# Performance work log

Hardware: AMD Instinct MI355X
Metric: run time of the kernel (lower is better)

The kernel has to match this reference:

```python
import jax, jax.numpy as jnp
import numpy as np

# Mamba2Simple defaults for Mamba2Simple(768, headdim=64)
D_MODEL = 768
D_STATE = 128
D_CONV = 4
EXPAND = 2
HEADDIM = 64
D_INNER = EXPAND * D_MODEL           # 1536
NHEADS = D_INNER // HEADDIM          # 24
CONV_DIM = D_INNER + 2 * D_STATE     # 1792 (x, B, C share the depthwise conv)
D_IN_PROJ = 2 * D_INNER + 2 * D_STATE + NHEADS  # 3352 (z, xBC, dt)
N_LAYERS = 4
IM8 = 64      # 8x8 image tokens
IM64 = 4096   # 64x64 image tokens
L = 1 + IM8 + IM64  # 4161 = s0 + im8 + zoom(im8)
B = 4
EPS = 1e-5


def setup_inputs() -> dict:
    key = jax.random.key(0)
    ks = iter(jax.random.split(key, 40))
    nrm = lambda shape, s=0.02: jax.random.normal(next(ks), shape, jnp.float32) * s
    inp = {
        'im8': jax.random.normal(next(ks), (B, IM8, 3), jnp.float32),
        'im64': jax.random.normal(next(ks), (B, IM64, 3), jnp.float32),
        # RGBToModel / ModelToRGB linear projections
        'from_rgb_w': nrm((3, D_MODEL)),
        'from_rgb_b': jnp.zeros((D_MODEL,), jnp.float32),
        'to_rgb_w': nrm((D_MODEL, 3)),
        'to_rgb_b': jnp.zeros((3,), jnp.float32),
        # learned prefix token and zoom positional suffix
        's0': nrm((1, 1, D_MODEL), 1.0),
        'suffix': nrm((IM64, D_MODEL), 1.0),
        'norm0_w': jnp.ones((D_MODEL,), jnp.float32),
        'norm0_b': jnp.zeros((D_MODEL,), jnp.float32),
        # per-layer (stacked over N_LAYERS) Mamba2 params
        'ln_w': jnp.ones((N_LAYERS, D_MODEL), jnp.float32),
        'ln_b': jnp.zeros((N_LAYERS, D_MODEL), jnp.float32),
        'in_proj_w': nrm((N_LAYERS, D_MODEL, D_IN_PROJ)),
        'conv_w': nrm((N_LAYERS, CONV_DIM, D_CONV), 0.1),
        'conv_b': jnp.zeros((N_LAYERS, CONV_DIM), jnp.float32),
        'dt_bias': nrm((N_LAYERS, NHEADS), 0.1),
        'A_log': jnp.log(jax.random.uniform(next(ks), (N_LAYERS, NHEADS), jnp.float32, 1.0, 16.0)),
        'D': nrm((N_LAYERS, NHEADS), 1.0),
        'gn_w': jnp.ones((N_LAYERS, D_INNER), jnp.float32),
        'out_proj_w': nrm((N_LAYERS, D_INNER, D_MODEL)),
    }
    return inp


def _layernorm(x, w, b):
    mu = jnp.mean(x, axis=-1, keepdims=True)
    var = jnp.mean((x - mu) ** 2, axis=-1, keepdims=True)
    return (x - mu) * jax.lax.rsqrt(var + EPS) * w + b


def _rmsnorm(x, w):
    return x * jax.lax.rsqrt(jnp.mean(x * x, axis=-1, keepdims=True) + EPS) * w


def _causal_conv1d(x, w, b):
    # x: (B, L, C) depthwise causal conv, kernel (C, K)
    xt = x.transpose(0, 2, 1)  # (B, C, L)
    y = jax.lax.conv_general_dilated(
        xt, w[:, None, :], window_strides=(1,), padding=[(D_CONV - 1, 0)],
        dimension_numbers=('NCH', 'OIH', 'NCH'), feature_group_count=w.shape[0])
    return y.transpose(0, 2, 1) + b


def _mamba2(u, Wi, cw, cb, dtb, Alog, Dh, gw, Wo):
    # u: (B, L, d_model)
    Bsz, Ln, _ = u.shape
    zxbcdt = u @ Wi  # (B, L, D_IN_PROJ)
    z = zxbcdt[..., :D_INNER]
    xBC = zxbcdt[..., D_INNER:D_INNER + CONV_DIM]
    dt = jax.nn.softplus(zxbcdt[..., D_INNER + CONV_DIM:] + dtb)  # (B, L, H)
    xBC = jax.nn.silu(_causal_conv1d(xBC, cw, cb))
    x = xBC[..., :D_INNER].reshape(Bsz, Ln, NHEADS, HEADDIM)  # (B,L,H,P)
    Bm = xBC[..., D_INNER:D_INNER + D_STATE]                  # (B,L,N)
    Cm = xBC[..., D_INNER + D_STATE:]                         # (B,L,N)
    A = -jnp.exp(Alog)            # (H,)
    dA = jnp.exp(dt * A)          # (B,L,H) decay factors

    def step(state, inputs):
        # state: (B,H,P,N)
        xt, dtt, dAt, Bt, Ct = inputs
        state = state * dAt[:, :, None, None] + jnp.einsum('bh,bhp,bn->bhpn', dtt, xt, Bt)
        y = jnp.einsum('bhpn,bn->bhp', state, Ct)
        return state, y

    st0 = jnp.zeros((Bsz, NHEADS, HEADDIM, D_STATE), u.dtype)
    xs = (x.transpose(1, 0, 2, 3), dt.transpose(1, 0, 2), dA.transpose(1, 0, 2),
          Bm.transpose(1, 0, 2), Cm.transpose(1, 0, 2))
    _, ys = jax.lax.scan(step, st0, xs)  # ys: (L,B,H,P)
    y = ys.transpose(1, 0, 2, 3) + Dh[None, None, :, None] * x  # D skip per head
    y = y.reshape(Bsz, Ln, D_INNER)
    y = _rmsnorm(y * jax.nn.silu(z), gw)  # RMSNormGated (norm_before_gate=False)
    return y @ Wo


def reference(im8, im64, from_rgb_w, from_rgb_b, to_rgb_w, to_rgb_b, s0, suffix,
              norm0_w, norm0_b, ln_w, ln_b, in_proj_w, conv_w, conv_b,
              dt_bias, A_log, D, gn_w, out_proj_w):
    Bsz = im8.shape[0]
    h8 = im8 @ from_rgb_w + from_rgb_b  # (B,64,d)
    # zoom: each 8x8 pixel repeated into an 8x8 block -> 64x64, plus suffix
    v = h8.reshape(Bsz, 8, 8, D_MODEL)
    zm = jnp.repeat(jnp.repeat(v, 8, axis=1), 8, axis=2).reshape(Bsz, IM64, D_MODEL) + suffix
    x = jnp.concatenate([jnp.broadcast_to(s0, (Bsz, 1, D_MODEL)), h8, zm], axis=1)  # (B,4161,d)
    x = _layernorm(x, norm0_w, norm0_b)
    for i in range(N_LAYERS):
        x = x + _mamba2(_layernorm(x, ln_w[i], ln_b[i]), in_proj_w[i], conv_w[i],
                        conv_b[i], dt_bias[i], A_log[i], D[i], gn_w[i], out_proj_w[i])
    x = x[:, -IM64:]
    y_hat = x @ to_rgb_w + to_rgb_b  # (B,4096,3)
    loss = jnp.mean((y_hat - im64) ** 2)
    return y_hat, loss
```

## Files before the change

kernel.cpp:

```cpp
#include <hip/hip_runtime.h>
#include <hip/hip_bf16.h>
#include <math.h>

#define LTOT 4161
#define BATCH 4
#define NROWS (BATCH*LTOT)
#define NPAD1 3456
#define DM 768
#define DI 1536
#define DIP 3352
#define ZLD 3328
#define NH 24
#define HD 64
#define DS 128
#define EPSF 1e-5f
#define CHK 128
#define NCH 33
#define NBLK (BATCH*NCH*NH)
#define LDF 136
#define XLD 72
#define RLD 264

typedef __attribute__((ext_vector_type(8))) __bf16 bf16x8;
typedef __attribute__((ext_vector_type(4))) float f32x4;
typedef __attribute__((ext_vector_type(8))) short short8;
typedef __attribute__((ext_vector_type(4))) unsigned int u32x4;
typedef unsigned short u16;
typedef unsigned int u32;

static __device__ __forceinline__ u16 f2bf(float f){
  unsigned u = __builtin_bit_cast(unsigned, f);
  u += 0x7FFFu + ((u >> 16) & 1u);
  return (u16)(u >> 16);
}
static __device__ __forceinline__ float bf2f(u16 v){
  return __builtin_bit_cast(float, ((unsigned)v) << 16);
}
static __device__ __forceinline__ float siluf(float v){ return v / (1.f + __expf(-v)); }

static __device__ __forceinline__ int xcd_swz(int orig, int nwg){
  int xcd = orig & 7;
  int idx = orig >> 3;
  int q = nwg >> 3, r = nwg & 7;
  int base = (xcd < r) ? xcd*(q + 1) : r*(q + 1) + (xcd - r)*q;
  return base + idx;
}

__device__ __forceinline__ float blockSum256(float v, float* sh){
  #pragma unroll
  for (int o = 32; o > 0; o >>= 1) v += __shfl_down(v, o);
  int w = threadIdx.x >> 6;
  if ((threadIdx.x & 63) == 0) sh[w] = v;
  __syncthreads();
  v = sh[0] + sh[1] + sh[2] + sh[3];
  __syncthreads();
  return v;
}

__global__ __launch_bounds__(256)
void build_x_kernel(const float* __restrict__ im8, const float* __restrict__ frw,
                    const float* __restrict__ frb, const float* __restrict__ s0,
                    const float* __restrict__ suffix, const float* __restrict__ w,
                    const float* __restrict__ bb, float* __restrict__ x)
{
  int row = blockIdx.x;
  int b = row / LTOT, l = row % LTOT;
  int t = threadIdx.x;
  __shared__ float sh[4];
  float v[3];
  if (l == 0) {
    #pragma unroll
    for (int i = 0; i < 3; i++) v[i] = s0[t + i*256];
  } else if (l <= 64) {
    int p = l - 1;
    float r0 = im8[(b*64 + p)*3 + 0], r1 = im8[(b*64 + p)*3 + 1], r2 = im8[(b*64 + p)*3 + 2];
    #pragma unroll
    for (int i = 0; i < 3; i++) {
      int d = t + i*256;
      v[i] = r0*frw[d] + r1*frw[768 + d] + r2*frw[1536 + d] + frb[d];
    }
  } else {
    int j = l - 65;
    int p = ((j >> 9) << 3) | ((j & 63) >> 3);
    float r0 = im8[(b*64 + p)*3 + 0], r1 = im8[(b*64 + p)*3 + 1], r2 = im8[(b*64 + p)*3 + 2];
    #pragma unroll
    for (int i = 0; i < 3; i++) {
      int d = t + i*256;
      v[i] = r0*frw[d] + r1*frw[768 + d] + r2*frw[1536 + d] + frb[d] + suffix[(size_t)j*768 + d];
    }
  }
  float s = v[0] + v[1] + v[2];
  s = blockSum256(s, sh);
  float mu = s * (1.f/768.f);
  float q = 0;
  #pragma unroll
  for (int i = 0; i < 3; i++) { float d = v[i] - mu; q += d*d; }
  q = blockSum256(q, sh);
  float rs = rsqrtf(q * (1.f/768.f) + EPSF);
  float* xr = x + (size_t)row*DM;
  #pragma unroll
  for (int i = 0; i < 3; i++) {
    int d = t + i*256;
    xr[d] = (v[i] - mu)*rs*w[d] + bb[d];
  }
}

__global__ __launch_bounds__(256)
void ln_bf16_kernel(const float* __restrict__ x, const float* __restrict__ w,
                    const float* __restrict__ bb, u16* __restrict__ out,
                    float* __restrict__ ssq)
{
  int row = blockIdx.x;
  int t = threadIdx.x;
  __shared__ float sh[4];
  const float* xr = x + (size_t)row*DM;
  float v[3];
  #pragma unroll
  for (int i = 0; i < 3; i++) v[i] = xr[t + i*256];
  if (t == 0) ssq[row] = 0.f;
  float s = v[0] + v[1] + v[2];
  s = blockSum256(s, sh);
  float mu = s * (1.f/768.f);
  float q = 0;
  #pragma unroll
  for (int i = 0; i < 3; i++) { float d = v[i] - mu; q += d*d; }
  q = blockSum256(q, sh);
  float rs = rsqrtf(q * (1.f/768.f) + EPSF);
  u16* orow = out + (size_t)row*DM;
  #pragma unroll
  for (int i = 0; i < 3; i++) {
    int d = t + i*256;
    orow[d] = f2bf((v[i] - mu)*rs*w[d] + bb[d]);
  }
}

__global__ __launch_bounds__(256)
void transp_bf16(const float* __restrict__ in, u16* __restrict__ out, int K, int N)
{
  __shared__ float tl[32][33];
  int tx = threadIdx.x & 31, ty = threadIdx.x >> 5;
  int n0 = blockIdx.x * 32, k0 = blockIdx.y * 32;
  #pragma unroll
  for (int r = 0; r < 4; r++) {
    int k = k0 + ty + r*8, n = n0 + tx;
    tl[ty + r*8][tx] = (n < N) ? in[(size_t)k*N + n] : 0.f;
  }
  __syncthreads();
  #pragma unroll
  for (int r = 0; r < 4; r++) {
    int n = n0 + ty + r*8, k = k0 + tx;
    out[(size_t)n*K + k] = f2bf(tl[tx][ty + r*8]);
  }
}

#define LD8(p) (*(const short8*)(p))

__global__ __launch_bounds__(256)
void gemm0(const u16* __restrict__ A, const u16* __restrict__ BT,
           u16* __restrict__ zxO, const float* __restrict__ dtbias,
           float* __restrict__ dtO)
{
  __shared__ __align__(16) u16 As[2][128*40];
  __shared__ __align__(16) u16 Bs[2][128*40];
  const int t = threadIdx.x;
  const int nid = xcd_swz(blockIdx.y*27 + blockIdx.x, 27*131);
  const int bm = nid / 27, bn = nid % 27;
  const int lane = t & 63, wave = t >> 6;
  const int wr = wave >> 1, wc = wave & 1;
  const int r16 = lane & 15, kb = lane >> 4;

  const int m = t >> 1, half = t & 1;
  const int grow = bm*128 + m;
  const bool valid = grow < NROWS;
  const u16* gA = A + (size_t)(valid ? grow : 0)*DM + half*16;
  const u16* gB = BT + (size_t)(bn*128 + m)*DM + half*16;
  const int wofs = m*40 + half*16;

  short8 a0 = {}, a1 = {}, b0, b1;
  b0 = LD8(gB); b1 = LD8(gB + 8);
  if (valid) { a0 = LD8(gA); a1 = LD8(gA + 8); }
  *(short8*)&As[0][wofs] = a0; *(short8*)&As[0][wofs + 8] = a1;
  *(short8*)&Bs[0][wofs] = b0; *(short8*)&Bs[0][wofs + 8] = b1;
  __syncthreads();

  f32x4 acc[4][4] = {};
  int p = 0;
  for (int kt = 0; kt < DM; kt += 32) {
    const bool more = (kt + 32 < DM);
    if (more) {
      b0 = LD8(gB + kt + 32); b1 = LD8(gB + kt + 40);
      if (valid) { a0 = LD8(gA + kt + 32); a1 = LD8(gA + kt + 40); }
    }
    bf16x8 af[4], bfr[4];
    #pragma unroll
    for (int i = 0; i < 4; i++) af[i]  = *(const bf16x8*)&As[p][(wr*64 + i*16 + r16)*40 + kb*8];
    #pragma unroll
    for (int i = 0; i < 4; i++) bfr[i] = *(const bf16x8*)&Bs[p][(wc*64 + i*16 + r16)*40 + kb*8];
    #pragma unroll
    for (int i = 0; i < 4; i++)
      #pragma unroll
      for (int j = 0; j < 4; j++)
        acc[i][j] = __builtin_amdgcn_mfma_f32_16x16x32_bf16(af[i], bfr[j], acc[i][j], 0, 0, 0);
    if (more) {
      *(short8*)&As[p^1][wofs] = a0; *(short8*)&As[p^1][wofs + 8] = a1;
      *(short8*)&Bs[p^1][wofs] = b0; *(short8*)&Bs[p^1][wofs + 8] = b1;
    }
    __syncthreads();
    p ^= 1;
  }
  const int rbase = bm*128 + wr*64, cbase = bn*128 + wc*64;
  #pragma unroll
  for (int i = 0; i < 4; i++) {
    #pragma unroll
    for (int j = 0; j < 4; j++) {
      int col = cbase + j*16 + r16;
      #pragma unroll
      for (int e = 0; e < 4; e++) {
        int row = rbase + i*16 + kb*4 + e;
        if (row < NROWS) {
          float v = acc[i][j][e];
          if (col < ZLD) {
            zxO[(size_t)row*ZLD + col] = f2bf(v);
          } else if (col < DIP) {
            int hh = col - ZLD;
            float d = v + dtbias[hh];
            d = (d > 20.f) ? d : log1pf(expf(d));
            dtO[(size_t)row*NH + hh] = d;
          }
        }
      }
    }
  }
}

__global__ __launch_bounds__(256)
void gemm_out(const u16* __restrict__ A, const float* __restrict__ ssq,
              const float* __restrict__ gw, const u16* __restrict__ BT,
              float* __restrict__ X)
{
  __shared__ __align__(16) u16 As[2][128*40];
  __shared__ __align__(16) u16 Bs[2][128*40];
  __shared__ float gwl[DI];
  const int t = threadIdx.x;
  const int nid = xcd_swz(blockIdx.y*6 + blockIdx.x, 6*131);
  const int bm = nid / 6, bn = nid % 6;
  const int lane = t & 63, wave = t >> 6;
  const int wr = wave >> 1, wc = wave & 1;
  const int r16 = lane & 15, kb = lane >> 4;

  for (int i = t; i < DI; i += 256) gwl[i] = gw[i];

  const int m = t >> 1, half = t & 1;
  const int grow = bm*128 + m;
  const bool valid = grow < NROWS;
  const float rs = valid ? rsqrtf(ssq[grow] * (1.f/1536.f) + EPSF) : 0.f;
  const u16* gA = A + (size_t)(valid ? grow : 0)*ZLD + half*16;
  const u16* gB = BT + (size_t)(bn*128 + m)*DI + half*16;
  const int wofs = m*40 + half*16;

  short8 ra0 = {}, ra1 = {}, b0, b1;
  b0 = LD8(gB); b1 = LD8(gB + 8);
  if (valid) { ra0 = LD8(gA); ra1 = LD8(gA + 8); }
  __syncthreads();
  {
    const int c0 = half*16;
    short8 ta0, ta1;
    #pragma unroll
    for (int j = 0; j < 8; j++) ta0[j] = (short)f2bf(bf2f((u16)ra0[j]) * rs * gwl[c0 + j]);
    #pragma unroll
    for (int j = 0; j < 8; j++) ta1[j] = (short)f2bf(bf2f((u16)ra1[j]) * rs * gwl[c0 + 8 + j]);
    *(short8*)&As[0][wofs] = ta0; *(short8*)&As[0][wofs + 8] = ta1;
    *(short8*)&Bs[0][wofs] = b0;  *(short8*)&Bs[0][wofs + 8] = b1;
  }
  __syncthreads();

  f32x4 acc[4][4] = {};
  int p = 0;
  for (int kt = 0; kt < DI; kt += 32) {
    const bool more = (kt + 32 < DI);
    if (more) {
      b0 = LD8(gB + kt + 32); b1 = LD8(gB + kt + 40);
      if (valid) { ra0 = LD8(gA + kt + 32); ra1 = LD8(gA + kt + 40); }
    }
    bf16x8 af[4], bfr[4];
    #pragma unroll
    for (int i = 0; i < 4; i++) af[i]  = *(const bf16x8*)&As[p][(wr*64 + i*16 + r16)*40 + kb*8];
    #pragma unroll
    for (int i = 0; i < 4; i++) bfr[i] = *(const bf16x8*)&Bs[p][(wc*64 + i*16 + r16)*40 + kb*8];
    #pragma unroll
    for (int i = 0; i < 4; i++)
      #pragma unroll
      for (int j = 0; j < 4; j++)
        acc[i][j] = __builtin_amdgcn_mfma_f32_16x16x32_bf16(af[i], bfr[j], acc[i][j], 0, 0, 0);
    if (more) {
      const int c0 = kt + 32 + half*16;
      short8 ta0, ta1;
      #pragma unroll
      for (int j = 0; j < 8; j++) ta0[j] = (short)f2bf(bf2f((u16)ra0[j]) * rs * gwl[c0 + j]);
      #pragma unroll
      for (int j = 0; j < 8; j++) ta1[j] = (short)f2bf(bf2f((u16)ra1[j]) * rs * gwl[c0 + 8 + j]);
      *(short8*)&As[p^1][wofs] = ta0; *(short8*)&As[p^1][wofs + 8] = ta1;
      *(short8*)&Bs[p^1][wofs] = b0;  *(short8*)&Bs[p^1][wofs + 8] = b1;
    }
    __syncthreads();
    p ^= 1;
  }
  const int rbase = bm*128 + wr*64, cbase = bn*128 + wc*64;
  #pragma unroll
  for (int i = 0; i < 4; i++) {
    #pragma unroll
    for (int j = 0; j < 4; j++) {
      int col = cbase + j*16 + r16;
      #pragma unroll
      for (int e = 0; e < 4; e++) {
        int row = rbase + i*16 + kb*4 + e;
        if (row < NROWS) X[(size_t)row*DM + col] += acc[i][j][e];
      }
    }
  }
}


__global__ __launch_bounds__(128)
void dtcs_kernel(const float* __restrict__ dt, const float* __restrict__ alog,
                 float* __restrict__ csb, float* __restrict__ dtvb,
                 float* __restrict__ wjsb, float* __restrict__ dtot)
{
  const int id = blockIdx.x;
  const int h = id % NH; const int c = (id / NH) % NCH; const int b = id / (NH*NCH);
  const int t = threadIdx.x;
  const int base = c*CHK;
  int rows = LTOT - base; if (rows > CHK) rows = CHK;
  __shared__ float cs[128];
  float dv = 0.f;
  if (t < rows) dv = dt[(size_t)(b*LTOT + base + t)*NH + h];
  const float aexp = __expf(alog[h]);
  cs[t] = -dv * aexp;
  __syncthreads();
  for (int off = 1; off < 128; off <<= 1) {
    float add = (t >= off) ? cs[t - off] : 0.f;
    __syncthreads();
    cs[t] += add;
    __syncthreads();
  }
  float csl = cs[127];
  size_t o = (size_t)id*128 + t;
  csb[o] = cs[t];
  dtvb[o] = dv;
  wjsb[o] = __expf(csl - cs[t]) * dv;
  if (t == 0) dtot[id] = __expf(csl);
}

__global__ __launch_bounds__(256)
void convBC_kernel(const u16* __restrict__ zx, const float* __restrict__ cw,
                   const float* __restrict__ cb, u16* __restrict__ Ccv,
                   u16* __restrict__ BcvT, u16* __restrict__ Sraw)
{
  const int bc = xcd_swz(blockIdx.x, BATCH*NCH);
  const int b = bc / NCH, c = bc % NCH;
  const int t = threadIdx.x;
  const int base = c*CHK;
  __shared__ __align__(16) u16 raw[131*RLD + 8];
  __shared__ __align__(16) u16 Bt[128*LDF];
  __shared__ __align__(16) u16 Ct[128*LDF];
  const u16* zb = zx + (size_t)(b*LTOT)*ZLD;

  #pragma unroll
  for (int rg = 0; rg < 17; rg++) {
    int idx = rg*256 + t;
    int r = idx >> 5, seg = idx & 31;
    if (r < 131) {
      int g = base - 3 + r;
      short8 v = {};
      if (g >= 0 && g < LTOT) v = LD8(zb + (size_t)g*ZLD + 3072 + seg*8);
      *(short8*)&raw[r*RLD + seg*8] = v;
    }
  }
  __syncthreads();
  {
    const int isC = t >> 7, n = t & 127;
    const int ch = 1536 + t;
    float w0 = cw[ch*4+0], w1 = cw[ch*4+1], w2 = cw[ch*4+2], w3 = cw[ch*4+3];
    float bias = cb[ch];
    float r0 = bf2f(raw[0*RLD + t]);
    float r1 = bf2f(raw[1*RLD + t]);
    float r2 = bf2f(raw[2*RLD + t]);
    u16* dstT = isC ? Ct : Bt;
    #pragma unroll 4
    for (int j = 0; j < 128; j++) {
      float r3 = bf2f(raw[(j + 3)*RLD + t]);
      float o = bias + w0*r0 + w1*r1 + w2*r2 + w3*r3;
      dstT[j*LDF + n] = f2bf(siluf(o));
      r0 = r1; r1 = r2; r2 = r3;
    }
  }
  __syncthreads();
  #pragma unroll
  for (int rg = 0; rg < 8; rg++) {
    int idx = rg*256 + t;
    int r = idx >> 4, seg = idx & 15;
    int g = base + r;
    if (g < LTOT)
      *(short8*)(Ccv + (size_t)(b*LTOT + g)*128 + seg*8) = *(const short8*)&Ct[r*LDF + seg*8];
  }
  u16* bT = BcvT + (size_t)bc*16384;
  #pragma unroll
  for (int rg = 0; rg < 8; rg++) {
    int idx = rg*256 + t;
    int n = idx >> 4, js = (idx & 15)*8;
    short8 v;
    #pragma unroll
    for (int k = 0; k < 8; k++) v[k] = (short)Bt[(js + k)*LDF + n];
    *(short8*)(bT + n*128 + js) = v;
  }
  {
    const int lane = t & 63, wave = t >> 6;
    const int r16 = lane & 15, kb = lane >> 4;
    f32x4 acc[2][8] = {};
    #pragma unroll
    for (int kt = 0; kt < 4; kt++) {
      bf16x8 af[2], bfr[8];
      #pragma unroll
      for (int m2 = 0; m2 < 2; m2++) af[m2] = *(const bf16x8*)&Ct[(wave*32 + m2*16 + r16)*LDF + kt*32 + kb*8];
      #pragma unroll
      for (int nj = 0; nj < 8; nj++) bfr[nj] = *(const bf16x8*)&Bt[(nj*16 + r16)*LDF + kt*32 + kb*8];
      #pragma unroll
      for (int m2 = 0; m2 < 2; m2++)
        #pragma unroll
        for (int nj = 0; nj < 8; nj++)
          acc[m2][nj] = __builtin_amdgcn_mfma_f32_16x16x32_bf16(af[m2], bfr[nj], acc[m2][nj], 0, 0, 0);
    }
    u16* sdst = Sraw + (size_t)bc*16384;
    #pragma unroll
    for (int m2 = 0; m2 < 2; m2++)
      #pragma unroll
      for (int nj = 0; nj < 8; nj++)
        #pragma unroll
        for (int e = 0; e < 4; e++) {
          int i = wave*32 + m2*16 + kb*4 + e;
          int j = nj*16 + r16;
          sdst[i*128 + j] = f2bf(acc[m2][nj][e]);
        }
  }
}

__global__ __launch_bounds__(256)
void chunk_state_kernel(const u16* __restrict__ zx, const float* __restrict__ wjsb,
                        const float* __restrict__ cw, const float* __restrict__ cb,
                        const u16* __restrict__ BcvT, u16* __restrict__ cstat)
{
  const int id = xcd_swz(blockIdx.x, NBLK);
  const int h = id % NH; const int c = (id / NH) % NCH; const int b = id / (NH*NCH);
  const int t = threadIdx.x;
  const int base = c*CHK;

  __shared__ __align__(16) u16 Bbuf[128*LDF];
  __shared__ __align__(16) u16 xbuf[131*XLD + 8];
  __shared__ float wjs[128];

  const u16* zb = zx + (size_t)(b*LTOT)*ZLD;
  if (t < 128) wjs[t] = wjsb[(size_t)id*128 + t];
  {
    const u16* bT = BcvT + (size_t)(b*NCH + c)*16384;
    #pragma unroll
    for (int rg = 0; rg < 8; rg++) {
      int idx = rg*256 + t;
      int n = idx >> 4, js = (idx & 15)*8;
      *(short8*)&Bbuf[n*LDF + js] = LD8(bT + n*128 + js);
    }
  }
  #pragma unroll
  for (int rg = 0; rg < 5; rg++) {
    int r = rg*32 + (t >> 3);
    int seg = t & 7;
    if (r < 131) {
      int g = base - 3 + r;
      short8 v = {};
      if (g >= 0 && g < LTOT) v = LD8(zb + (size_t)g*ZLD + 1536 + h*HD + seg*8);
      *(short8*)&xbuf[r*XLD + seg*8] = v;
    }
  }
  __syncthreads();

  const int p_ = t & 63, jq = t >> 6;
  u32 pkx[16];
  {
    const int ch = h*HD + p_;
    float w0 = cw[ch*4+0], w1 = cw[ch*4+1], w2 = cw[ch*4+2], w3 = cw[ch*4+3];
    float bias = cb[ch];
    const int rb = jq*32;
    float r0 = bf2f(xbuf[(rb+0)*XLD + p_]);
    float r1 = bf2f(xbuf[(rb+1)*XLD + p_]);
    float r2 = bf2f(xbuf[(rb+2)*XLD + p_]);
    #pragma unroll
    for (int k2 = 0; k2 < 16; k2++) {
      float r3 = bf2f(xbuf[(rb + 2*k2 + 3)*XLD + p_]);
      float o0 = bias + w0*r0 + w1*r1 + w2*r2 + w3*r3;
      float r4 = bf2f(xbuf[(rb + 2*k2 + 4)*XLD + p_]);
      float o1 = bias + w0*r1 + w1*r2 + w2*r3 + w3*r4;
      float s0 = siluf(o0) * wjs[rb + 2*k2];
      float s1 = siluf(o1) * wjs[rb + 2*k2 + 1];
      pkx[k2] = (u32)f2bf(s0) | ((u32)f2bf(s1) << 16);
      r0 = r2; r1 = r3; r2 = r4;
    }
  }
  __syncthreads();
  #pragma unroll
  for (int q = 0; q < 4; q++) {
    u32x4 v; v[0] = pkx[q*4]; v[1] = pkx[q*4+1]; v[2] = pkx[q*4+2]; v[3] = pkx[q*4+3];
    *(u32x4*)&xbuf[p_*LDF + jq*32 + q*8] = v;
  }
  __syncthreads();

  const int lane = t & 63, wave = t >> 6;
  const int r16 = lane & 15, kb = lane >> 4;
  const int n0 = wave*32;
  f32x4 acc[4][2] = {};
  #pragma unroll
  for (int kt = 0; kt < 4; kt++) {
    bf16x8 af[4], bfr[2];
    #pragma unroll
    for (int m = 0; m < 4; m++) af[m] = *(const bf16x8*)&xbuf[(m*16 + r16)*LDF + kt*32 + kb*8];
    #pragma unroll
    for (int nn = 0; nn < 2; nn++) bfr[nn] = *(const bf16x8*)&Bbuf[(n0 + nn*16 + r16)*LDF + kt*32 + kb*8];
    #pragma unroll
    for (int m = 0; m < 4; m++)
      #pragma unroll
      for (int nn = 0; nn < 2; nn++)
        acc[m][nn] = __builtin_amdgcn_mfma_f32_16x16x32_bf16(af[m], bfr[nn], acc[m][nn], 0, 0, 0);
  }
  u16* dst = cstat + (size_t)id*64*128;
  #pragma unroll
  for (int m = 0; m < 4; m++)
    #pragma unroll
    for (int nn = 0; nn < 2; nn++)
      #pragma unroll
      for (int e = 0; e < 4; e++) {
        int p = m*16 + kb*4 + e;
        int n = n0 + nn*16 + r16;
        dst[p*128 + n] = f2bf(acc[m][nn][e]);
      }
}

__global__ __launch_bounds__(256)
void state_scan_kernel(u16* __restrict__ cstat, const float* __restrict__ dtot)
{
  const int b = blockIdx.x / NH, h = blockIdx.x % NH;
  const int t = threadIdx.x;
  float run[32];
  #pragma unroll
  for (int k = 0; k < 32; k++) run[k] = 0.f;
  size_t id0 = (size_t)(b*NCH)*NH + h;
  short8 cur[4];
  {
    const u16* s0 = cstat + id0*8192 + t*32;
    #pragma unroll
    for (int q = 0; q < 4; q++) cur[q] = LD8(s0 + q*8);
  }
  float d = dtot[id0];
  for (int c = 0; c < NCH; ++c) {
    size_t id = (size_t)(b*NCH + c)*NH + h;
    u16* slab = cstat + id*8192 + t*32;
    short8 nxt[4] = {}; float nd = 0.f;
    if (c + 1 < NCH) {
      const u16* sn = slab + (size_t)NH*8192;
      #pragma unroll
      for (int q = 0; q < 4; q++) nxt[q] = LD8(sn + q*8);
      nd = dtot[id + NH];
    }
    short8 out[4];
    #pragma unroll
    for (int q = 0; q < 4; q++)
      #pragma unroll
      for (int k = 0; k < 8; k++) {
        int idx = q*8 + k;
        float csv = bf2f((u16)cur[q][k]);
        out[q][k] = (short)f2bf(run[idx]);
        run[idx] = run[idx]*d + csv;
      }
    #pragma unroll
    for (int q = 0; q < 4; q++) *(short8*)(slab + q*8) = out[q];
    #pragma unroll
    for (int q = 0; q < 4; q++) cur[q] = nxt[q];
    d = nd;
  }
}

__global__ __launch_bounds__(512, 4)
void chunk_output_kernel(u16* __restrict__ zx, const float* __restrict__ csb,
                         const float* __restrict__ dtvb, const float* __restrict__ cw,
                         const float* __restrict__ cb, const float* __restrict__ Dvec,
                         const u16* __restrict__ Sraw, const u16* __restrict__ Ccv,
                         const u16* __restrict__ cstat, float* __restrict__ ssq)
{
  const int id = xcd_swz(blockIdx.x, NBLK);
  const int h = id % NH; const int c = (id / NH) % NCH; const int b = id / (NH*NCH);
  const int t = threadIdx.x;
  const int base = c*CHK;
  int rows = LTOT - base; if (rows > CHK) rows = CHK;

  __shared__ __align__(16) u16 Bc[128*LDF];
  __shared__ __align__(16) u16 stT[64*LDF];
  __shared__ __align__(16) u16 xbuf[131*XLD + 8];
  __shared__ float dtv[128];
  __shared__ float cs[128];

  const u16* zb = zx + (size_t)(b*LTOT)*ZLD;
  const size_t crow0 = (size_t)(b*LTOT)*128;
  if (t < 128) {
    cs[t]  = csb[(size_t)id*128 + t];
    dtv[t] = dtvb[(size_t)id*128 + t];
  }
  {
    const u16* slab = cstat + (size_t)id*8192;
    int p = t >> 3, nb = (t & 7)*16;
    *(short8*)&stT[p*LDF + nb]     = LD8(slab + p*128 + nb);
    *(short8*)&stT[p*LDF + nb + 8] = LD8(slab + p*128 + nb + 8);
  }
  #pragma unroll
  for (int rg = 0; rg < 3; rg++) {
    int r = rg*64 + (t >> 3);
    int seg = t & 7;
    if (r < 131) {
      int g = base - 3 + r;
      short8 v = {};
      if (g >= 0 && g < LTOT) v = LD8(zb + (size_t)g*ZLD + 1536 + h*HD + seg*8);
      *(short8*)&xbuf[r*XLD + seg*8] = v;
    }
  }
  __syncthreads();

  const int p_ = t & 63, jq = t >> 6;
  u32 pkx[8];
  {
    const int ch = h*HD + p_;
    float w0 = cw[ch*4+0], w1 = cw[ch*4+1], w2 = cw[ch*4+2], w3 = cw[ch*4+3];
    float bias = cb[ch];
    const int rb = jq*16;
    float r0 = bf2f(xbuf[(rb+0)*XLD + p_]);
    float r1 = bf2f(xbuf[(rb+1)*XLD + p_]);
    float r2 = bf2f(xbuf[(rb+2)*XLD + p_]);
    #pragma unroll
    for (int k2 = 0; k2 < 8; k2++) {
      float r3 = bf2f(xbuf[(rb + 2*k2 + 3)*XLD + p_]);
      float o0 = bias + w0*r0 + w1*r1 + w2*r2 + w3*r3;
      float r4 = bf2f(xbuf[(rb + 2*k2 + 4)*XLD + p_]);
      float o1 = bias + w0*r1 + w1*r2 + w2*r3 + w3*r4;
      int j0 = rb + 2*k2;
      u32 lo = (j0     < rows) ? (u32)f2bf(siluf(o0)) : 0u;
      u32 hi = (j0 + 1 < rows) ? (u32)f2bf(siluf(o1)) : 0u;
      pkx[k2] = lo | (hi << 16);
      r0 = r2; r1 = r3; r2 = r4;
    }
  }
  {
    const u16* sS = Sraw + (size_t)(b*NCH + c)*16384;
    #pragma unroll
    for (int q = 0; q < 4; q++) {
      int idx = q*512 + t;
      int i = idx >> 4, seg = (idx & 15)*8;
      short8 s = LD8(sS + i*128 + seg);
      float csi = cs[i];
      short8 o;
      #pragma unroll
      for (int k = 0; k < 8; k++) {
        int j = seg + k;
        float f = 0.f;
        if (j <= i && i < rows) f = __expf(csi - cs[j]) * dtv[j];
        o[k] = (short)f2bf(bf2f((u16)s[k]) * f);
      }
      *(short8*)&Bc[i*LDF + seg] = o;
    }
  }
  __syncthreads();
  {
    u32x4 v0; v0[0] = pkx[0]; v0[1] = pkx[1]; v0[2] = pkx[2]; v0[3] = pkx[3];
    u32x4 v1; v1[0] = pkx[4]; v1[1] = pkx[5]; v1[2] = pkx[6]; v1[3] = pkx[7];
    *(u32x4*)&xbuf[p_*LDF + jq*16]     = v0;
    *(u32x4*)&xbuf[p_*LDF + jq*16 + 8] = v1;
  }
  __syncthreads();

  const int lane = t & 63, wave = t >> 6;
  const int r16 = lane & 15, kb = lane >> 4;

  {
    const int iq = wave;
    bf16x8 cF[4];
    {
      int i = iq*16 + r16;
      int g = base + i; if (g >= LTOT) g = base;
      #pragma unroll
      for (int kt = 0; kt < 4; kt++)
        cF[kt] = *(const bf16x8*)(Ccv + crow0 + (size_t)g*128 + kt*32 + kb*8);
    }
    f32x4 accY[4] = {};
    #pragma unroll
    for (int kt = 0; kt < 4; kt++) {
      bf16x8 af = *(const bf16x8*)&Bc[(iq*16 + r16)*LDF + kt*32 + kb*8];
      #pragma unroll
      for (int n = 0; n < 4; n++) {
        bf16x8 bfr = *(const bf16x8*)&xbuf[(n*16 + r16)*LDF + kt*32 + kb*8];
        accY[n] = __builtin_amdgcn_mfma_f32_16x16x32_bf16(af, bfr, accY[n], 0, 0, 0);
      }
    }
    f32x4 accS[4] = {};
    #pragma unroll
    for (int kt = 0; kt < 4; kt++) {
      #pragma unroll
      for (int n = 0; n < 4; n++) {
        bf16x8 bfr = *(const bf16x8*)&stT[(n*16 + r16)*LDF + kt*32 + kb*8];
        accS[n] = __builtin_amdgcn_mfma_f32_16x16x32_bf16(cF[kt], bfr, accS[n], 0, 0, 0);
      }
    }
    const float dcoef = Dvec[h];
    #pragma unroll
    for (int e = 0; e < 4; e++) {
      int i = iq*16 + kb*4 + e;
      if (i < rows) {
        float sc = __expf(cs[i]);
        size_t orow = (size_t)(b*LTOT + base + i)*ZLD + h*HD;
        float g2 = 0.f;
        #pragma unroll
        for (int n = 0; n < 4; n++) {
          int p = n*16 + r16;
          float xv = bf2f(xbuf[p*LDF + i]);
          float yv = accY[n][e] + sc*accS[n][e] + dcoef*xv;
          float gv = yv * siluf(bf2f(zx[orow + p]));
          zx[orow + p] = f2bf(gv);
          g2 += gv*gv;
        }
        g2 += __shfl_xor(g2, 1);
        g2 += __shfl_xor(g2, 2);
        g2 += __shfl_xor(g2, 4);
        g2 += __shfl_xor(g2, 8);
        if (r16 == 0) atomicAdd(&ssq[b*LTOT + base + i], g2);
      }
    }
  }
}

__global__ __launch_bounds__(256)
void head_kernel(const float* __restrict__ x, const float* __restrict__ tw,
                 const float* __restrict__ tb, const float* __restrict__ im64,
                 float* __restrict__ out, float* __restrict__ partial)
{
  int bj = blockIdx.x;
  int b = bj >> 12, j = bj & 4095;
  int row = b*LTOT + 65 + j;
  const float* xr = x + (size_t)row*DM;
  int t = threadIdx.x;
  float p0 = 0, p1 = 0, p2 = 0;
  for (int k = t; k < 768; k += 256) {
    float xv = xr[k];
    p0 += xv*tw[k*3 + 0]; p1 += xv*tw[k*3 + 1]; p2 += xv*tw[k*3 + 2];
  }
  __shared__ float sh[4];
  p0 = blockSum256(p0, sh);
  p1 = blockSum256(p1, sh);
  p2 = blockSum256(p2, sh);
  if (t == 0) {
    float y0 = p0 + tb[0], y1 = p1 + tb[1], y2 = p2 + tb[2];
    size_t o = (size_t)bj*3;
    out[o] = y0; out[o + 1] = y1; out[o + 2] = y2;
    float d0 = y0 - im64[o], d1 = y1 - im64[o + 1], d2 = y2 - im64[o + 2];
    partial[bj] = d0*d0 + d1*d1 + d2*d2;
  }
}

__global__ __launch_bounds__(256)
void loss_reduce(const float* __restrict__ partial, float* __restrict__ out)
{
  int t = threadIdx.x;
  float s = 0.f;
  for (int i = t; i < BATCH*4096; i += 256) s += partial[i];
  __shared__ float sh[4];
  s = blockSum256(s, sh);
  if (t == 0) out[49152] = s * (1.f/49152.f);
}

static inline size_t alignup(size_t v){ return (v + 255) & ~(size_t)255; }

extern "C" void kernel_launch(void* const* d_in, const int* in_sizes, int n_in,
                              void* d_out, int out_size, void* d_ws, size_t ws_size,
                              hipStream_t stream)
{
  const float* im8        = (const float*)d_in[0];
  const float* im64       = (const float*)d_in[1];
  const float* from_rgb_w = (const float*)d_in[2];
  const float* from_rgb_b = (const float*)d_in[3];
  const float* to_rgb_w   = (const float*)d_in[4];
  const float* to_rgb_b   = (const float*)d_in[5];
  const float* s0         = (const float*)d_in[6];
  const float* suffix     = (const float*)d_in[7];
  const float* norm0_w    = (const float*)d_in[8];
  const float* norm0_b    = (const float*)d_in[9];
  const float* ln_w       = (const float*)d_in[10];
  const float* ln_b       = (const float*)d_in[11];
  const float* in_proj_w  = (const float*)d_in[12];
  const float* conv_w     = (const float*)d_in[13];
  const float* conv_b     = (const float*)d_in[14];
  const float* dt_bias    = (const float*)d_in[15];
  const float* A_log      = (const float*)d_in[16];
  const float* Dvec       = (const float*)d_in[17];
  const float* gn_w       = (const float*)d_in[18];
  const float* out_proj_w = (const float*)d_in[19];

  char* w = (char*)d_ws;
  size_t off = 0;
  float* x     = (float*)(w + off); off = alignup(off + (size_t)NROWS*DM*4);
  u16*   zx    = (u16*)  (w + off); off = alignup(off + (size_t)NROWS*ZLD*2);
  u16*   scr   = (u16*)  (w + off); off = alignup(off + (size_t)NBLK*64*128*2);
  u16*   Sraw  = (u16*)  (w + off); off = alignup(off + (size_t)BATCH*NCH*16384*2);
  u16*   Ccv   = (u16*)  (w + off); off = alignup(off + (size_t)NROWS*128*2);
  u16*   BcvT  = (u16*)  (w + off); off = alignup(off + (size_t)BATCH*NCH*16384*2);
  float* dt    = (float*)(w + off); off = alignup(off + (size_t)NROWS*NH*4);
  float* csb   = (float*)(w + off); off = alignup(off + (size_t)NBLK*128*4);
  float* dtvb  = (float*)(w + off); off = alignup(off + (size_t)NBLK*128*4);
  float* wjsb  = (float*)(w + off); off = alignup(off + (size_t)NBLK*128*4);
  float* ssq   = (float*)(w + off); off = alignup(off + (size_t)NROWS*4);
  float* dtot  = (float*)(w + off); off = alignup(off + (size_t)NBLK*4);
  float* lpart = (float*)(w + off); off = alignup(off + (size_t)BATCH*4096*4);
  u16* wT    = scr;
  u16* xn    = (u16*)((char*)scr + alignup((size_t)NPAD1*DM*2));
  u16* cstat = scr;

  build_x_kernel<<<NROWS, 256, 0, stream>>>(im8, from_rgb_w, from_rgb_b, s0, suffix,
                                            norm0_w, norm0_b, x);

  for (int i = 0; i < 4; i++) {
    ln_bf16_kernel<<<NROWS, 256, 0, stream>>>(x, ln_w + i*DM, ln_b + i*DM, xn, ssq);
    transp_bf16<<<dim3(NPAD1/32, DM/32), 256, 0, stream>>>(in_proj_w + (size_t)i*DM*DIP, wT, DM, DIP);
    gemm0<<<dim3(27, 131), 256, 0, stream>>>(xn, wT, zx, dt_bias + i*NH, dt);
    dtcs_kernel<<<NBLK, 128, 0, stream>>>(dt, A_log + i*NH, csb, dtvb, wjsb, dtot);
    convBC_kernel<<<BATCH*NCH, 256, 0, stream>>>(zx, conv_w + (size_t)i*(DI+2*DS)*4,
        conv_b + i*(DI+2*DS), Ccv, BcvT, Sraw);
    chunk_state_kernel<<<NBLK, 256, 0, stream>>>(zx, wjsb,
        conv_w + (size_t)i*(DI+2*DS)*4, conv_b + i*(DI+2*DS), BcvT, cstat);
    state_scan_kernel<<<BATCH*NH, 256, 0, stream>>>(cstat, dtot);
    chunk_output_kernel<<<NBLK, 512, 0, stream>>>(zx, csb, dtvb,
        conv_w + (size_t)i*(DI+2*DS)*4, conv_b + i*(DI+2*DS), Dvec + i*NH, Sraw, Ccv, cstat, ssq);
    transp_bf16<<<dim3(DM/32, DI/32), 256, 0, stream>>>(out_proj_w + (size_t)i*DI*DM, wT, DI, DM);
    gemm_out<<<dim3(6, 131), 256, 0, stream>>>(zx, ssq, gn_w + i*DI, wT, x);
  }

  head_kernel<<<BATCH*4096, 256, 0, stream>>>(x, to_rgb_w, to_rgb_b, im64, (float*)d_out, lpart);
  loss_reduce<<<1, 256, 0, stream>>>(lpart, (float*)d_out);
}
```

Before: 2.130 ms.

## Widen convBC to 512 threads and split state scan across four blocks per head

convBC_kernel now runs 512 threads per block. Each channel's causal conv is split into two 64-row halves, and each wave computes a 16-row strip of the C·Bᵀ MFMA product. state_scan_kernel launches four times as many blocks, each handling one quarter of the 64x128 state slab with 8 elements per thread instead of 32. Both changes add parallelism to small-grid kernels (132 and 96 blocks) that left most CUs idle. The cost is more redundant conv-weight loads and more blocks each re-reading the per-chunk decay factors.

```diff
diff --git a/kernel.cpp b/kernel.cpp
--- a/kernel.cpp
+++ b/kernel.cpp
@@ -351,7 +351,7 @@
   if (t == 0) dtot[id] = __expf(csl);
 }
 
-__global__ __launch_bounds__(256)
+__global__ __launch_bounds__(512)
 void convBC_kernel(const u16* __restrict__ zx, const float* __restrict__ cw,
                    const float* __restrict__ cb, u16* __restrict__ Ccv,
                    u16* __restrict__ BcvT, u16* __restrict__ Sraw)
@@ -366,8 +366,8 @@
   const u16* zb = zx + (size_t)(b*LTOT)*ZLD;
 
   #pragma unroll
-  for (int rg = 0; rg < 17; rg++) {
-    int idx = rg*256 + t;
+  for (int rg = 0; rg < 9; rg++) {
+    int idx = rg*512 + t;
     int r = idx >> 5, seg = idx & 31;
     if (r < 131) {
       int g = base - 3 + r;
@@ -378,26 +378,28 @@
   }
   __syncthreads();
   {
-    const int isC = t >> 7, n = t & 127;
-    const int ch = 1536 + t;
+    const int cht = t & 255, halfj = t >> 8;
+    const int isC = cht >> 7, n = cht & 127;
+    const int ch = 1536 + cht;
     float w0 = cw[ch*4+0], w1 = cw[ch*4+1], w2 = cw[ch*4+2], w3 = cw[ch*4+3];
     float bias = cb[ch];
-    float r0 = bf2f(raw[0*RLD + t]);
-    float r1 = bf2f(raw[1*RLD + t]);
-    float r2 = bf2f(raw[2*RLD + t]);
+    const int rb = halfj*64;
+    float r0 = bf2f(raw[(rb+0)*RLD + cht]);
+    float r1 = bf2f(raw[(rb+1)*RLD + cht]);
+    float r2 = bf2f(raw[(rb+2)*RLD + cht]);
     u16* dstT = isC ? Ct : Bt;
     #pragma unroll 4
-    for (int j = 0; j < 128; j++) {
-      float r3 = bf2f(raw[(j + 3)*RLD + t]);
+    for (int j = 0; j < 64; j++) {
+      float r3 = bf2f(raw[(rb + j + 3)*RLD + cht]);
       float o = bias + w0*r0 + w1*r1 + w2*r2 + w3*r3;
-      dstT[j*LDF + n] = f2bf(siluf(o));
+      dstT[(rb + j)*LDF + n] = f2bf(siluf(o));
       r0 = r1; r1 = r2; r2 = r3;
     }
   }
   __syncthreads();
   #pragma unroll
-  for (int rg = 0; rg < 8; rg++) {
-    int idx = rg*256 + t;
+  for (int rg = 0; rg < 4; rg++) {
+    int idx = rg*512 + t;
     int r = idx >> 4, seg = idx & 15;
     int g = base + r;
     if (g < LTOT)
@@ -405,8 +407,8 @@
   }
   u16* bT = BcvT + (size_t)bc*16384;
   #pragma unroll
-  for (int rg = 0; rg < 8; rg++) {
-    int idx = rg*256 + t;
+  for (int rg = 0; rg < 4; rg++) {
+    int idx = rg*512 + t;
     int n = idx >> 4, js = (idx & 15)*8;
     short8 v;
     #pragma unroll
@@ -416,31 +418,25 @@
   {
     const int lane = t & 63, wave = t >> 6;
     const int r16 = lane & 15, kb = lane >> 4;
-    f32x4 acc[2][8] = {};
+    f32x4 acc[8] = {};
     #pragma unroll
     for (int kt = 0; kt < 4; kt++) {
-      bf16x8 af[2], bfr[8];
-      #pragma unroll
-      for (int m2 = 0; m2 < 2; m2++) af[m2] = *(const bf16x8*)&Ct[(wave*32 + m2*16 + r16)*LDF + kt*32 + kb*8];
-      #pragma unroll
-      for (int nj = 0; nj < 8; nj++) bfr[nj] = *(const bf16x8*)&Bt[(nj*16 + r16)*LDF + kt*32 + kb*8];
-      #pragma unroll
-      for (int m2 = 0; m2 < 2; m2++)
-        #pragma unroll
-        for (int nj = 0; nj < 8; nj++)
-          acc[m2][nj] = __builtin_amdgcn_mfma_f32_16x16x32_bf16(af[m2], bfr[nj], acc[m2][nj], 0, 0, 0);
+      bf16x8 af = *(const bf16x8*)&Ct[(wave*16 + r16)*LDF + kt*32 + kb*8];
+      #pragma unroll
+      for (int nj = 0; nj < 8; nj++) {
+        bf16x8 bfr = *(const bf16x8*)&Bt[(nj*16 + r16)*LDF + kt*32 + kb*8];
+        acc[nj] = __builtin_amdgcn_mfma_f32_16x16x32_bf16(af, bfr, acc[nj], 0, 0, 0);
+      }
     }
     u16* sdst = Sraw + (size_t)bc*16384;
     #pragma unroll
-    for (int m2 = 0; m2 < 2; m2++)
-      #pragma unroll
-      for (int nj = 0; nj < 8; nj++)
-        #pragma unroll
-        for (int e = 0; e < 4; e++) {
-          int i = wave*32 + m2*16 + kb*4 + e;
-          int j = nj*16 + r16;
-          sdst[i*128 + j] = f2bf(acc[m2][nj][e]);
-        }
+    for (int nj = 0; nj < 8; nj++)
+      #pragma unroll
+      for (int e = 0; e < 4; e++) {
+        int i = wave*16 + kb*4 + e;
+        int j = nj*16 + r16;
+        sdst[i*128 + j] = f2bf(acc[nj][e]);
+      }
   }
 }
 
@@ -545,43 +541,35 @@
 __global__ __launch_bounds__(256)
 void state_scan_kernel(u16* __restrict__ cstat, const float* __restrict__ dtot)
 {
-  const int b = blockIdx.x / NH, h = blockIdx.x % NH;
+  const int blk = blockIdx.x;
+  const int b = blk / (NH*4);
+  const int rest = blk % (NH*4);
+  const int h = rest >> 2, sec = rest & 3;
   const int t = threadIdx.x;
-  float run[32];
-  #pragma unroll
-  for (int k = 0; k < 32; k++) run[k] = 0.f;
+  const int eofs = sec*2048 + t*8;
+  float run[8];
+  #pragma unroll
+  for (int k = 0; k < 8; k++) run[k] = 0.f;
   size_t id0 = (size_t)(b*NCH)*NH + h;
-  short8 cur[4];
-  {
-    const u16* s0 = cstat + id0*8192 + t*32;
-    #pragma unroll
-    for (int q = 0; q < 4; q++) cur[q] = LD8(s0 + q*8);
-  }
+  short8 cur = LD8(cstat + id0*8192 + eofs);
   float d = dtot[id0];
   for (int c = 0; c < NCH; ++c) {
     size_t id = (size_t)(b*NCH + c)*NH + h;
-    u16* slab = cstat + id*8192 + t*32;
-    short8 nxt[4] = {}; float nd = 0.f;
+    u16* slab = cstat + id*8192 + eofs;
+    short8 nxt = {}; float nd = 0.f;
     if (c + 1 < NCH) {
-      const u16* sn = slab + (size_t)NH*8192;
-      #pragma unroll
-      for (int q = 0; q < 4; q++) nxt[q] = LD8(sn + q*8);
+      nxt = LD8(slab + (size_t)NH*8192);
       nd = dtot[id + NH];
     }
-    short8 out[4];
-    #pragma unroll
-    for (int q = 0; q < 4; q++)
-      #pragma unroll
-      for (int k = 0; k < 8; k++) {
-        int idx = q*8 + k;
-        float csv = bf2f((u16)cur[q][k]);
-        out[q][k] = (short)f2bf(run[idx]);
-        run[idx] = run[idx]*d + csv;
-      }
-    #pragma unroll
-    for (int q = 0; q < 4; q++) *(short8*)(slab + q*8) = out[q];
-    #pragma unroll
-    for (int q = 0; q < 4; q++) cur[q] = nxt[q];
+    short8 out;
+    #pragma unroll
+    for (int k = 0; k < 8; k++) {
+      float csv = bf2f((u16)cur[k]);
+      out[k] = (short)f2bf(run[k]);
+      run[k] = run[k]*d + csv;
+    }
+    *(short8*)slab = out;
+    cur = nxt;
     d = nd;
   }
 }
@@ -833,11 +821,11 @@
     transp_bf16<<<dim3(NPAD1/32, DM/32), 256, 0, stream>>>(in_proj_w + (size_t)i*DM*DIP, wT, DM, DIP);
     gemm0<<<dim3(27, 131), 256, 0, stream>>>(xn, wT, zx, dt_bias + i*NH, dt);
     dtcs_kernel<<<NBLK, 128, 0, stream>>>(dt, A_log + i*NH, csb, dtvb, wjsb, dtot);
-    convBC_kernel<<<BATCH*NCH, 256, 0, stream>>>(zx, conv_w + (size_t)i*(DI+2*DS)*4,
+    convBC_kernel<<<BATCH*NCH, 512, 0, stream>>>(zx, conv_w + (size_t)i*(DI+2*DS)*4,
         conv_b + i*(DI+2*DS), Ccv, BcvT, Sraw);
     chunk_state_kernel<<<NBLK, 256, 0, stream>>>(zx, wjsb,
         conv_w + (size_t)i*(DI+2*DS)*4, conv_b + i*(DI+2*DS), BcvT, cstat);
-    state_scan_kernel<<<BATCH*NH, 256, 0, stream>>>(cstat, dtot);
+    state_scan_kernel<<<BATCH*NH*4, 256, 0, stream>>>(cstat, dtot);
     chunk_output_kernel<<<NBLK, 512, 0, stream>>>(zx, csb, dtvb,
         conv_w + (size_t)i*(DI+2*DS)*4, conv_b + i*(DI+2*DS), Dvec + i*NH, Sraw, Ccv, cstat, ssq);
     transp_bf16<<<dim3(DM/32, DI/32), 256, 0, stream>>>(out_proj_w + (size_t)i*DI*DM, wT, DI, DM);
```

Result: faster. 1.986 ms (-6.7%).
